# Kernel tuning notes

Hardware: AMD Instinct MI355X
Metric: run time of the kernel (lower is better)

The kernel has to match this reference:

```python
import jax, jax.numpy as jnp
import numpy as np

N_NODES = 50000
DEG = 16            # fixed average degree -> nnz = N_NODES * DEG
NNZ = N_NODES * DEG
IN_FEATS = 256
OUT_FEATS = 128


def setup_inputs() -> dict:
    key = jax.random.key(0)
    k1, k2, k3, k4, k5, k6, k7 = jax.random.split(key, 7)
    # CSR adjacency: regular DEG edges per row (row_ptr strictly valid)
    row_ptr_s = (jnp.arange(N_NODES + 1, dtype=jnp.int32) * DEG)
    col_idx_s = jax.random.randint(k1, (NNZ,), 0, N_NODES, dtype=jnp.int32)
    edge_val_csr_s = jax.random.uniform(k2, (NNZ,), dtype=jnp.float32)
    # CSC copy (used only by the original CUDA backward kernel; plausible dummies)
    col_ptr_s = (jnp.arange(N_NODES + 1, dtype=jnp.int32) * DEG)
    row_idx_s = jax.random.randint(k3, (NNZ,), 0, N_NODES, dtype=jnp.int32)
    edge_val_csc_s = jax.random.uniform(k4, (NNZ,), dtype=jnp.float32)
    in_feat = jax.random.normal(k5, (N_NODES, IN_FEATS), dtype=jnp.float32)
    # Parameters: xavier-uniform W, zero bias
    limit = float(np.sqrt(6.0 / (IN_FEATS + OUT_FEATS)))
    W = jax.random.uniform(k6, (IN_FEATS, OUT_FEATS), dtype=jnp.float32,
                           minval=-limit, maxval=limit)
    bias = jnp.zeros((OUT_FEATS,), dtype=jnp.float32)
    return {
        "nnz": NNZ,
        "row_ptr_s": row_ptr_s, "col_idx_s": col_idx_s, "edge_val_csr_s": edge_val_csr_s,
        "p_csr": 1, "q_csr": 1,
        "col_ptr_s": col_ptr_s, "row_idx_s": row_idx_s, "edge_val_csc_s": edge_val_csc_s,
        "p_csc": 1, "q_csc": 1,
        "in_feat": in_feat, "W": W, "bias": bias,
    }


def _csr_spmm(row_ptr, col_idx, edge_val, h):
    """out[i] = sum_{e in row i} edge_val[e] * h[col_idx[e]]  (A @ h, A in CSR)."""
    n = row_ptr.shape[0] - 1
    nnz = col_idx.shape[0]
    # map each edge to its destination row via the row pointer
    row_id = jnp.searchsorted(row_ptr, jnp.arange(nnz, dtype=row_ptr.dtype), side="right") - 1
    msg = h[col_idx] * edge_val[:, None]          # [nnz, out_feats]
    return jax.ops.segment_sum(msg, row_id, num_segments=n)


def reference(nnz, row_ptr_s, col_idx_s, edge_val_csr_s, p_csr, q_csr,
              col_ptr_s, row_idx_s, edge_val_csc_s, p_csc, q_csc,
              in_feat, W, bias):
    h = in_feat @ W                                # [N, out_feats]
    rst = _csr_spmm(row_ptr_s, col_idx_s, edge_val_csr_s, h)
    return jax.nn.relu(rst + bias)
```

## Files before the change

### kernel.cpp

```cpp
#include <hip/hip_runtime.h>
#include <hip/hip_bf16.h>

#define IN_F 256
#define OUT_F 128
#define BM 32
#define GEMM_THREADS 512
#define GEMM_BLOCKS 512

typedef __bf16 bf16x8 __attribute__((ext_vector_type(8)));
typedef float  f32x4  __attribute__((ext_vector_type(4)));
typedef int    i32x4  __attribute__((ext_vector_type(4)));

__global__ __launch_bounds__(128)
void wprep_kernel(const float* __restrict__ W, __bf16* __restrict__ Wt)
{
    const int k = blockIdx.x;
    const int nn = threadIdx.x;
    Wt[nn * IN_F + k] = (__bf16)W[k * OUT_F + nn];
}

__global__ __launch_bounds__(GEMM_THREADS)
void gemm_xw_kernel(const float* __restrict__ X, const __bf16* __restrict__ Wt,
                    __bf16* __restrict__ H, int n, int ntiles)
{
    __shared__ __bf16 xs[2][BM * IN_F];

    const int tid  = threadIdx.x;
    const int lane = tid & 63;
    const int wid  = tid >> 6;
    const int wm   = wid >> 2;
    const int wn   = wid & 3;

    bf16x8 bfrag[8][2];
    {
        const int nbase = wn * 32 + (lane & 15);
        const int kbase = (lane >> 4) * 8;
        #pragma unroll
        for (int kk = 0; kk < 8; ++kk) {
            #pragma unroll
            for (int nf = 0; nf < 2; ++nf) {
                const __bf16* p = Wt + (size_t)(nbase + nf * 16) * IN_F + kk * 32 + kbase;
                bfrag[kk][nf] = *(const bf16x8*)p;
            }
        }
    }

    const int srow = tid >> 5;
    const int sk   = (tid & 31) * 8;

    int tile = blockIdx.x;
    if (tile < ntiles) {
        const int r0 = tile * BM;
        float4 a0 = make_float4(0,0,0,0), a1 = a0, b0 = a0, b1 = a0;
        const int gr0 = r0 + srow, gr1 = r0 + srow + 16;
        if (gr0 < n) {
            a0 = *(const float4*)(X + (size_t)gr0 * IN_F + sk);
            a1 = *(const float4*)(X + (size_t)gr0 * IN_F + sk + 4);
        }
        if (gr1 < n) {
            b0 = *(const float4*)(X + (size_t)gr1 * IN_F + sk);
            b1 = *(const float4*)(X + (size_t)gr1 * IN_F + sk + 4);
        }
        bf16x8 v0, v1;
        v0[0]=(__bf16)a0.x; v0[1]=(__bf16)a0.y; v0[2]=(__bf16)a0.z; v0[3]=(__bf16)a0.w;
        v0[4]=(__bf16)a1.x; v0[5]=(__bf16)a1.y; v0[6]=(__bf16)a1.z; v0[7]=(__bf16)a1.w;
        v1[0]=(__bf16)b0.x; v1[1]=(__bf16)b0.y; v1[2]=(__bf16)b0.z; v1[3]=(__bf16)b0.w;
        v1[4]=(__bf16)b1.x; v1[5]=(__bf16)b1.y; v1[6]=(__bf16)b1.z; v1[7]=(__bf16)b1.w;
        *(bf16x8*)&xs[0][(srow * IN_F + sk) ^ ((srow & 7) << 3)] = v0;
        *(bf16x8*)&xs[0][((srow + 16) * IN_F + sk) ^ (((srow + 16) & 7) << 3)] = v1;
    }
    __syncthreads();

    int cur = 0;
    for (; tile < ntiles; tile += gridDim.x) {
        const int nxt = tile + (int)gridDim.x;
        const bool has_next = nxt < ntiles;

        float4 a0 = make_float4(0,0,0,0), a1 = a0, b0 = a0, b1 = a0;
        if (has_next) {
            const int r0 = nxt * BM;
            const int gr0 = r0 + srow, gr1 = r0 + srow + 16;
            if (gr0 < n) {
                a0 = *(const float4*)(X + (size_t)gr0 * IN_F + sk);
                a1 = *(const float4*)(X + (size_t)gr0 * IN_F + sk + 4);
            }
            if (gr1 < n) {
                b0 = *(const float4*)(X + (size_t)gr1 * IN_F + sk);
                b1 = *(const float4*)(X + (size_t)gr1 * IN_F + sk + 4);
            }
        }

        f32x4 acc0 = (f32x4)0.f, acc1 = (f32x4)0.f;
        {
            const int arow  = wm * 16 + (lane & 15);
            const int akoff = (lane >> 4) * 8;
            #pragma unroll
            for (int kk = 0; kk < 8; ++kk) {
                const int sidx = (arow * IN_F + kk * 32 + akoff) ^ ((arow & 7) << 3);
                const bf16x8 a = *(const bf16x8*)&xs[cur][sidx];
                acc0 = __builtin_amdgcn_mfma_f32_16x16x32_bf16(a, bfrag[kk][0], acc0, 0, 0, 0);
                acc1 = __builtin_amdgcn_mfma_f32_16x16x32_bf16(a, bfrag[kk][1], acc1, 0, 0, 0);
            }
        }

        {
            const int crow0 = tile * BM + wm * 16 + (lane >> 4) * 4;
            const int ccol0 = wn * 32 + (lane & 15);
            #pragma unroll
            for (int j = 0; j < 4; ++j) {
                const int row = crow0 + j;
                if (row < n) {
                    H[(size_t)row * OUT_F + ccol0]      = (__bf16)acc0[j];
                    H[(size_t)row * OUT_F + ccol0 + 16] = (__bf16)acc1[j];
                }
            }
        }

        if (has_next) {
            bf16x8 v0, v1;
            v0[0]=(__bf16)a0.x; v0[1]=(__bf16)a0.y; v0[2]=(__bf16)a0.z; v0[3]=(__bf16)a0.w;
            v0[4]=(__bf16)a1.x; v0[5]=(__bf16)a1.y; v0[6]=(__bf16)a1.z; v0[7]=(__bf16)a1.w;
            v1[0]=(__bf16)b0.x; v1[1]=(__bf16)b0.y; v1[2]=(__bf16)b0.z; v1[3]=(__bf16)b0.w;
            v1[4]=(__bf16)b1.x; v1[5]=(__bf16)b1.y; v1[6]=(__bf16)b1.z; v1[7]=(__bf16)b1.w;
            const int nb = cur ^ 1;
            *(bf16x8*)&xs[nb][(srow * IN_F + sk) ^ ((srow & 7) << 3)] = v0;
            *(bf16x8*)&xs[nb][((srow + 16) * IN_F + sk) ^ (((srow + 16) & 7) << 3)] = v1;
        }
        __syncthreads();
        cur ^= 1;
    }
}

__global__ __launch_bounds__(256, 4)
void spmm_bias_relu_kernel(const int* __restrict__ row_ptr,
                           const int* __restrict__ col_idx,
                           const float* __restrict__ val,
                           const __bf16* __restrict__ H,
                           const float* __restrict__ bias,
                           float* __restrict__ out, int n)
{
    const int row = blockIdx.x * 16 + (threadIdx.x >> 4);
    const int c8  = (threadIdx.x & 15) * 8;
    if (row >= n) return;

    const int s = row_ptr[row];
    const int e = row_ptr[row + 1];

    const f32x4 b0 = *(const f32x4*)(bias + c8);
    const f32x4 b1 = *(const f32x4*)(bias + c8 + 4);

    float acc[8];
    #pragma unroll
    for (int j = 0; j < 8; ++j) acc[j] = 0.f;

    if (e - s == 16 && (s & 3) == 0) {
        i32x4 ci[4];
        f32x4 vi[4];
        #pragma unroll
        for (int i = 0; i < 4; ++i) {
            ci[i] = __builtin_nontemporal_load((const i32x4*)(col_idx + s) + i);
            vi[i] = __builtin_nontemporal_load((const f32x4*)(val + s) + i);
        }
        bf16x8 hv[16];
        #pragma unroll
        for (int i = 0; i < 16; ++i)
            hv[i] = *(const bf16x8*)(H + (size_t)ci[i >> 2][i & 3] * OUT_F + c8);
        #pragma unroll
        for (int i = 0; i < 16; ++i) {
            const float v = vi[i >> 2][i & 3];
            #pragma unroll
            for (int j = 0; j < 8; ++j)
                acc[j] = fmaf(v, (float)hv[i][j], acc[j]);
        }
    } else {
        for (int ee = s; ee < e; ++ee) {
            const int   col = col_idx[ee];
            const float v   = val[ee];
            const bf16x8 hv = *(const bf16x8*)(H + (size_t)col * OUT_F + c8);
            #pragma unroll
            for (int j = 0; j < 8; ++j)
                acc[j] = fmaf(v, (float)hv[j], acc[j]);
        }
    }

    f32x4 o0 = { fmaxf(acc[0] + b0[0], 0.f), fmaxf(acc[1] + b0[1], 0.f),
                 fmaxf(acc[2] + b0[2], 0.f), fmaxf(acc[3] + b0[3], 0.f) };
    f32x4 o1 = { fmaxf(acc[4] + b1[0], 0.f), fmaxf(acc[5] + b1[1], 0.f),
                 fmaxf(acc[6] + b1[2], 0.f), fmaxf(acc[7] + b1[3], 0.f) };
    __builtin_nontemporal_store(o0, (f32x4*)(out + (size_t)row * OUT_F + c8));
    __builtin_nontemporal_store(o1, (f32x4*)(out + (size_t)row * OUT_F + c8 + 4));
}

extern "C" void kernel_launch(void* const* d_in, const int* in_sizes, int n_in,
                              void* d_out, int out_size, void* d_ws, size_t ws_size,
                              hipStream_t stream)
{
    const int*   row_ptr = (const int*)  d_in[1];
    const int*   col_idx = (const int*)  d_in[2];
    const float* edgeval = (const float*)d_in[3];
    const float* in_feat = (const float*)d_in[11];
    const float* W       = (const float*)d_in[12];
    const float* bias    = (const float*)d_in[13];

    const int n = in_sizes[11] / IN_F;

    __bf16* H  = (__bf16*)d_ws;
    __bf16* Wt = (__bf16*)((char*)d_ws + (size_t)n * OUT_F * 2);

    wprep_kernel<<<IN_F, OUT_F, 0, stream>>>(W, Wt);

    const int ntiles = (n + BM - 1) / BM;
    const int gemm_blocks = ntiles < GEMM_BLOCKS ? ntiles : GEMM_BLOCKS;
    gemm_xw_kernel<<<gemm_blocks, GEMM_THREADS, 0, stream>>>(in_feat, Wt, H, n, ntiles);

    const int spmm_blocks = (n + 15) / 16;
    spmm_bias_relu_kernel<<<spmm_blocks, 256, 0, stream>>>(
        row_ptr, col_idx, edgeval, H, bias, (float*)d_out, n);
}
```

Measured before the change: 53.83 us.

## Drop LDS staging in GEMM; waves load X directly into MFMA fragments

The XW GEMM no longer stages X tiles through double-buffered shared memory with block barriers. Each wave now owns a 16-row stripe and a 32-column output slice, loading fp32 X straight from global memory into bf16 MFMA fragments, and the launch bounds request higher occupancy. This removes the LDS traffic and __syncthreads cost, but each X row is now read by four separate waves (one per column group), which relies on cache hits, and the loads are less coalesced and no longer prefetched.

```diff
diff --git a/kernel.cpp b/kernel.cpp
--- a/kernel.cpp
+++ b/kernel.cpp
@@ -3,7 +3,6 @@
 
 #define IN_F 256
 #define OUT_F 128
-#define BM 32
 #define GEMM_THREADS 512
 #define GEMM_BLOCKS 512
 
@@ -19,21 +18,20 @@
     Wt[nn * IN_F + k] = (__bf16)W[k * OUT_F + nn];
 }
 
-__global__ __launch_bounds__(GEMM_THREADS)
+__global__ __launch_bounds__(GEMM_THREADS, 3)
 void gemm_xw_kernel(const float* __restrict__ X, const __bf16* __restrict__ Wt,
-                    __bf16* __restrict__ H, int n, int ntiles)
+                    __bf16* __restrict__ H, int n, int nstripes)
 {
-    __shared__ __bf16 xs[2][BM * IN_F];
-
-    const int tid  = threadIdx.x;
-    const int lane = tid & 63;
-    const int wid  = tid >> 6;
-    const int wm   = wid >> 2;
-    const int wn   = wid & 3;
+    const int lane  = threadIdx.x & 63;
+    const int wid   = threadIdx.x >> 6;
+    const int gwave = blockIdx.x * (GEMM_THREADS / 64) + wid;
+    const int g     = gwave & 3;
+    const int s0    = gwave >> 2;
+    const int sstep = (GEMM_BLOCKS * (GEMM_THREADS / 64)) >> 2;
 
     bf16x8 bfrag[8][2];
     {
-        const int nbase = wn * 32 + (lane & 15);
+        const int nbase = g * 32 + (lane & 15);
         const int kbase = (lane >> 4) * 8;
         #pragma unroll
         for (int kk = 0; kk < 8; ++kk) {
@@ -45,89 +43,36 @@
         }
     }
 
-    const int srow = tid >> 5;
-    const int sk   = (tid & 31) * 8;
+    const int arow_off = lane & 15;
+    const int akoff    = (lane >> 4) * 8;
 
-    int tile = blockIdx.x;
-    if (tile < ntiles) {
-        const int r0 = tile * BM;
-        float4 a0 = make_float4(0,0,0,0), a1 = a0, b0 = a0, b1 = a0;
-        const int gr0 = r0 + srow, gr1 = r0 + srow + 16;
-        if (gr0 < n) {
-            a0 = *(const float4*)(X + (size_t)gr0 * IN_F + sk);
-            a1 = *(const float4*)(X + (size_t)gr0 * IN_F + sk + 4);
+    for (int s = s0; s < nstripes; s += sstep) {
+        const int r0 = s * 16;
+        const int arow = min(r0 + arow_off, n - 1);
+        const float* pX = X + (size_t)arow * IN_F + akoff;
+
+        f32x4 acc0 = (f32x4)0.f, acc1 = (f32x4)0.f;
+        #pragma unroll
+        for (int kk = 0; kk < 8; ++kk) {
+            const float4 x0 = *(const float4*)(pX + kk * 32);
+            const float4 x1 = *(const float4*)(pX + kk * 32 + 4);
+            bf16x8 a;
+            a[0]=(__bf16)x0.x; a[1]=(__bf16)x0.y; a[2]=(__bf16)x0.z; a[3]=(__bf16)x0.w;
+            a[4]=(__bf16)x1.x; a[5]=(__bf16)x1.y; a[6]=(__bf16)x1.z; a[7]=(__bf16)x1.w;
+            acc0 = __builtin_amdgcn_mfma_f32_16x16x32_bf16(a, bfrag[kk][0], acc0, 0, 0, 0);
+            acc1 = __builtin_amdgcn_mfma_f32_16x16x32_bf16(a, bfrag[kk][1], acc1, 0, 0, 0);
         }
-        if (gr1 < n) {
-            b0 = *(const float4*)(X + (size_t)gr1 * IN_F + sk);
-            b1 = *(const float4*)(X + (size_t)gr1 * IN_F + sk + 4);
-        }
-        bf16x8 v0, v1;
-        v0[0]=(__bf16)a0.x; v0[1]=(__bf16)a0.y; v0[2]=(__bf16)a0.z; v0[3]=(__bf16)a0.w;
-        v0[4]=(__bf16)a1.x; v0[5]=(__bf16)a1.y; v0[6]=(__bf16)a1.z; v0[7]=(__bf16)a1.w;
-        v1[0]=(__bf16)b0.x; v1[1]=(__bf16)b0.y; v1[2]=(__bf16)b0.z; v1[3]=(__bf16)b0.w;
-        v1[4]=(__bf16)b1.x; v1[5]=(__bf16)b1.y; v1[6]=(__bf16)b1.z; v1[7]=(__bf16)b1.w;
-        *(bf16x8*)&xs[0][(srow * IN_F + sk) ^ ((srow & 7) << 3)] = v0;
-        *(bf16x8*)&xs[0][((srow + 16) * IN_F + sk) ^ (((srow + 16) & 7) << 3)] = v1;
-    }
-    __syncthreads();
 
-    int cur = 0;
-    for (; tile < ntiles; tile += gridDim.x) {
-        const int nxt = tile + (int)gridDim.x;
-        const bool has_next = nxt < ntiles;
-
-        float4 a0 = make_float4(0,0,0,0), a1 = a0, b0 = a0, b1 = a0;
-        if (has_next) {
-            const int r0 = nxt * BM;
-            const int gr0 = r0 + srow, gr1 = r0 + srow + 16;
-            if (gr0 < n) {
-                a0 = *(const float4*)(X + (size_t)gr0 * IN_F + sk);
-                a1 = *(const float4*)(X + (size_t)gr0 * IN_F + sk + 4);
-            }
-            if (gr1 < n) {
-                b0 = *(const float4*)(X + (size_t)gr1 * IN_F + sk);
-                b1 = *(const float4*)(X + (size_t)gr1 * IN_F + sk + 4);
+        const int crow0 = r0 + (lane >> 4) * 4;
+        const int ccol0 = g * 32 + (lane & 15);
+        #pragma unroll
+        for (int j = 0; j < 4; ++j) {
+            const int row = crow0 + j;
+            if (row < n) {
+                H[(size_t)row * OUT_F + ccol0]      = (__bf16)acc0[j];
+                H[(size_t)row * OUT_F + ccol0 + 16] = (__bf16)acc1[j];
             }
         }
-
-        f32x4 acc0 = (f32x4)0.f, acc1 = (f32x4)0.f;
-        {
-            const int arow  = wm * 16 + (lane & 15);
-            const int akoff = (lane >> 4) * 8;
-            #pragma unroll
-            for (int kk = 0; kk < 8; ++kk) {
-                const int sidx = (arow * IN_F + kk * 32 + akoff) ^ ((arow & 7) << 3);
-                const bf16x8 a = *(const bf16x8*)&xs[cur][sidx];
-                acc0 = __builtin_amdgcn_mfma_f32_16x16x32_bf16(a, bfrag[kk][0], acc0, 0, 0, 0);
-                acc1 = __builtin_amdgcn_mfma_f32_16x16x32_bf16(a, bfrag[kk][1], acc1, 0, 0, 0);
-            }
-        }
-
-        {
-            const int crow0 = tile * BM + wm * 16 + (lane >> 4) * 4;
-            const int ccol0 = wn * 32 + (lane & 15);
-            #pragma unroll
-            for (int j = 0; j < 4; ++j) {
-                const int row = crow0 + j;
-                if (row < n) {
-                    H[(size_t)row * OUT_F + ccol0]      = (__bf16)acc0[j];
-                    H[(size_t)row * OUT_F + ccol0 + 16] = (__bf16)acc1[j];
-                }
-            }
-        }
-
-        if (has_next) {
-            bf16x8 v0, v1;
-            v0[0]=(__bf16)a0.x; v0[1]=(__bf16)a0.y; v0[2]=(__bf16)a0.z; v0[3]=(__bf16)a0.w;
-            v0[4]=(__bf16)a1.x; v0[5]=(__bf16)a1.y; v0[6]=(__bf16)a1.z; v0[7]=(__bf16)a1.w;
-            v1[0]=(__bf16)b0.x; v1[1]=(__bf16)b0.y; v1[2]=(__bf16)b0.z; v1[3]=(__bf16)b0.w;
-            v1[4]=(__bf16)b1.x; v1[5]=(__bf16)b1.y; v1[6]=(__bf16)b1.z; v1[7]=(__bf16)b1.w;
-            const int nb = cur ^ 1;
-            *(bf16x8*)&xs[nb][(srow * IN_F + sk) ^ ((srow & 7) << 3)] = v0;
-            *(bf16x8*)&xs[nb][((srow + 16) * IN_F + sk) ^ (((srow + 16) & 7) << 3)] = v1;
-        }
-        __syncthreads();
-        cur ^= 1;
     }
 }
 
@@ -209,9 +154,8 @@
 
     wprep_kernel<<<IN_F, OUT_F, 0, stream>>>(W, Wt);
 
-    const int ntiles = (n + BM - 1) / BM;
-    const int gemm_blocks = ntiles < GEMM_BLOCKS ? ntiles : GEMM_BLOCKS;
-    gemm_xw_kernel<<<gemm_blocks, GEMM_THREADS, 0, stream>>>(in_feat, Wt, H, n, ntiles);
+    const int nstripes = (n + 15) / 16;
+    gemm_xw_kernel<<<GEMM_BLOCKS, GEMM_THREADS, 0, stream>>>(in_feat, Wt, H, n, nstripes);
 
     const int spmm_blocks = (n + 15) / 16;
     spmm_bias_relu_kernel<<<spmm_blocks, 256, 0, stream>>>(
```

Result: slower. 71.72 us (+33.2%).
